# Kernel optimization log

Measured on AMD Instinct MI355X. Metric: run time of the kernel, lower is better.

Reference implementation:

```python
import jax, jax.numpy as jnp
import numpy as np
import math

N_EMBD = 1024
DIM_ATT = 1024
N_LAYER = 24
LAYER_ID = 12
B, T = 4, 4096


def _init_params():
    r01 = LAYER_ID / (N_LAYER - 1)
    r1a0 = 1.0 - LAYER_ID / N_LAYER
    ddd = np.arange(N_EMBD, dtype=np.float32) / N_EMBD
    h = np.arange(DIM_ATT, dtype=np.float32)
    decay_speed = -5.0 + 8.0 * (h / (DIM_ATT - 1)) ** (0.7 + 1.3 * r01)
    zigzag = (((np.arange(DIM_ATT) + 1) % 3) - 1).astype(np.float32) * 0.5
    time_first = np.float32(math.log(0.3)) + zigzag
    return {
        'time_decay': jnp.asarray(decay_speed, jnp.float32),
        'time_first': jnp.asarray(time_first, jnp.float32),
        'time_mix_k': jnp.asarray(ddd ** r1a0, jnp.float32),
        'time_mix_v': jnp.asarray(ddd ** r1a0 + 0.3 * r01, jnp.float32),
        'time_mix_r': jnp.asarray(ddd ** (0.5 * r1a0), jnp.float32),
    }


def setup_inputs() -> dict:
    key = jax.random.key(0)
    ks = jax.random.split(key, 5)
    inp = {'x': jax.random.normal(ks[0], (B, T, N_EMBD), jnp.float32)}
    inp.update(_init_params())
    s = 1.0 / math.sqrt(N_EMBD)
    inp['Wk'] = jax.random.normal(ks[1], (DIM_ATT, N_EMBD), jnp.float32) * s
    inp['Wv'] = jax.random.normal(ks[2], (DIM_ATT, N_EMBD), jnp.float32) * s
    inp['Wr'] = jax.random.normal(ks[3], (DIM_ATT, N_EMBD), jnp.float32) * s
    inp['Wo'] = jax.random.normal(ks[4], (N_EMBD, DIM_ATT), jnp.float32) * (1.0 / math.sqrt(DIM_ATT))
    return inp


def _wkv(w, u, k, v):
    # Numerically stable RWKV-4 WKV recurrence. w = -exp(time_decay) <= 0.
    # k, v: [B, T, C]; w, u: [C]. Scan over T with [B, C] state.
    def step(carry, kv):
        aa, bb, pp = carry
        kt, vt = kv
        ww = u + kt
        p = jnp.maximum(pp, ww)
        e1 = jnp.exp(pp - p)
        e2 = jnp.exp(ww - p)
        y = (e1 * aa + e2 * vt) / (e1 * bb + e2)
        ww2 = pp + w
        p2 = jnp.maximum(ww2, kt)
        e1b = jnp.exp(ww2 - p2)
        e2b = jnp.exp(kt - p2)
        return (e1b * aa + e2b * vt, e1b * bb + e2b, p2), y

    Bb, Tt, C = k.shape
    init = (jnp.zeros((Bb, C), k.dtype), jnp.zeros((Bb, C), k.dtype),
            jnp.full((Bb, C), -1e38, k.dtype))
    _, ys = jax.lax.scan(step, init, (jnp.swapaxes(k, 0, 1), jnp.swapaxes(v, 0, 1)))
    return jnp.swapaxes(ys, 0, 1)


def reference(x, time_decay, time_first, time_mix_k, time_mix_v, time_mix_r, Wk, Wv, Wr, Wo):
    # time_shift: ZeroPad2d((0,0,1,-1)) -> shift right by 1 along T with zero fill
    xx = jnp.pad(x, ((0, 0), (1, 0), (0, 0)))[:, :-1]
    xk = x * time_mix_k + xx * (1.0 - time_mix_k)
    xv = x * time_mix_v + xx * (1.0 - time_mix_v)
    xr = x * time_mix_r + xx * (1.0 - time_mix_r)
    k = jnp.einsum('btc,dc->btd', xk, Wk)
    v = jnp.einsum('btc,dc->btd', xv, Wv)
    sr = jax.nn.sigmoid(jnp.einsum('btc,dc->btd', xr, Wr))
    w = -jnp.exp(time_decay)  # as in the WKV CUDA kernel
    rwkv = sr * _wkv(w, time_first, k, v)
    return jnp.einsum('btd,cd->btc', rwkv, Wo)
```

## Files before the change

kernel.cpp:

```cpp
#include <hip/hip_runtime.h>
#include <hip/hip_bf16.h>
#include <stdint.h>

#define B_ 4
#define T_ 4096
#define C_ 1024
#define D_ 1024
#define NC_ 64
#define LC_ 64

typedef __bf16 bf16x8 __attribute__((ext_vector_type(8)));
typedef float  f32x4  __attribute__((ext_vector_type(4)));

__device__ __forceinline__ unsigned short f2bf(float f) {
    union { float f; unsigned u; } c; c.f = f;
    return (unsigned short)((c.u + 0x7fffu + ((c.u >> 16) & 1u)) >> 16);
}

__device__ __forceinline__ void gload_lds16(const unsigned short* g, unsigned short* l) {
    __builtin_amdgcn_global_load_lds(
        (const __attribute__((address_space(1))) void*)g,
        (__attribute__((address_space(3))) void*)l,
        16, 0, 0);
}

__global__ void cast_bf16_kernel(const float* __restrict__ s, unsigned short* __restrict__ d) {
    int i = blockIdx.x * blockDim.x + threadIdx.x;
    float4 v = *reinterpret_cast<const float4*>(s + ((size_t)i << 2));
    ushort4 o;
    o.x = f2bf(v.x); o.y = f2bf(v.y); o.z = f2bf(v.z); o.w = f2bf(v.w);
    *reinterpret_cast<ushort4*>(d + ((size_t)i << 2)) = o;
}

__global__ void mix_cast_kernel(const float* __restrict__ x,
                                const float* __restrict__ mk,
                                const float* __restrict__ mv,
                                const float* __restrict__ mr,
                                unsigned short* __restrict__ xk,
                                unsigned short* __restrict__ xv,
                                unsigned short* __restrict__ xr) {
    int i = blockIdx.x * blockDim.x + threadIdx.x;
    int base = i << 2;
    int c = base & (C_ - 1);
    int m = base >> 10;
    int t = m & (T_ - 1);
    float4 xc = *reinterpret_cast<const float4*>(x + base);
    float4 xp = make_float4(0.f, 0.f, 0.f, 0.f);
    if (t != 0) xp = *reinterpret_cast<const float4*>(x + base - C_);
    float4 k4 = *reinterpret_cast<const float4*>(mk + c);
    float4 v4 = *reinterpret_cast<const float4*>(mv + c);
    float4 r4 = *reinterpret_cast<const float4*>(mr + c);
    ushort4 ok, ov, orr;
    ok.x  = f2bf(xp.x + k4.x * (xc.x - xp.x));
    ok.y  = f2bf(xp.y + k4.y * (xc.y - xp.y));
    ok.z  = f2bf(xp.z + k4.z * (xc.z - xp.z));
    ok.w  = f2bf(xp.w + k4.w * (xc.w - xp.w));
    ov.x  = f2bf(xp.x + v4.x * (xc.x - xp.x));
    ov.y  = f2bf(xp.y + v4.y * (xc.y - xp.y));
    ov.z  = f2bf(xp.z + v4.z * (xc.z - xp.z));
    ov.w  = f2bf(xp.w + v4.w * (xc.w - xp.w));
    orr.x = f2bf(xp.x + r4.x * (xc.x - xp.x));
    orr.y = f2bf(xp.y + r4.y * (xc.y - xp.y));
    orr.z = f2bf(xp.z + r4.z * (xc.z - xp.z));
    orr.w = f2bf(xp.w + r4.w * (xc.w - xp.w));
    *reinterpret_cast<ushort4*>(xk + base) = ok;
    *reinterpret_cast<ushort4*>(xv + base) = ov;
    *reinterpret_cast<ushort4*>(xr + base) = orr;
}

template<bool SIG>
__global__ __launch_bounds__(256) void gemm_bt(const unsigned short* __restrict__ A,
                                               const unsigned short* __restrict__ Bw,
                                               float* __restrict__ Cm) {
    __shared__ __align__(16) unsigned short As[128 * 32];
    __shared__ __align__(16) unsigned short Bs[128 * 32];
    const int tid  = threadIdx.x;
    const int lane = tid & 63;
    const int wid  = tid >> 6;
    const int xcd   = blockIdx.x & 7;
    const int local = blockIdx.x >> 3;
    const int bm = (((xcd << 4) + (local >> 3))) << 7;
    const int bn = (local & 7) << 7;
    const int wr = (wid >> 1) * 64;
    const int wc = (wid & 1) * 64;

    f32x4 acc[4][4] = {};

    const int r0 = tid >> 2;
    const int ck = (tid & 3) * 8;
    const unsigned short* ga0 = A  + (size_t)(bm + r0) * 1024 + ck;
    const unsigned short* gb0 = Bw + (size_t)(bn + r0) * 1024 + ck;
    const unsigned short* ga1 = ga0 + (size_t)64 * 1024;
    const unsigned short* gb1 = gb0 + (size_t)64 * 1024;
    unsigned short* lA0 = As + wid * 512;
    unsigned short* lA1 = As + 2048 + wid * 512;
    unsigned short* lB0 = Bs + wid * 512;
    unsigned short* lB1 = Bs + 2048 + wid * 512;

    const int arow = wr + (lane & 15);
    const int brow = wc + (lane & 15);
    const int ko   = (lane >> 4) * 8;

    for (int ks = 0; ks < 32; ++ks) {
        __syncthreads();
        gload_lds16(ga0, lA0);
        gload_lds16(ga1, lA1);
        gload_lds16(gb0, lB0);
        gload_lds16(gb1, lB1);
        ga0 += 32; ga1 += 32; gb0 += 32; gb1 += 32;
        asm volatile("s_waitcnt vmcnt(0)" ::: "memory");
        __syncthreads();

        bf16x8 af[4], bfr[4];
        #pragma unroll
        for (int i = 0; i < 4; ++i) {
            af[i]  = *reinterpret_cast<const bf16x8*>(&As[(arow + i * 16) * 32 + ko]);
            bfr[i] = *reinterpret_cast<const bf16x8*>(&Bs[(brow + i * 16) * 32 + ko]);
        }
        #pragma unroll
        for (int i = 0; i < 4; ++i)
            #pragma unroll
            for (int j = 0; j < 4; ++j)
                acc[i][j] = __builtin_amdgcn_mfma_f32_16x16x32_bf16(af[i], bfr[j], acc[i][j], 0, 0, 0);
    }

    const int row0 = bm + wr + (lane >> 4) * 4;
    const int col0 = bn + wc + (lane & 15);
    #pragma unroll
    for (int i = 0; i < 4; ++i)
        #pragma unroll
        for (int j = 0; j < 4; ++j)
            #pragma unroll
            for (int r = 0; r < 4; ++r) {
                float vv = acc[i][j][r];
                if (SIG) vv = 1.0f / (1.0f + __expf(-vv));
                Cm[(size_t)(row0 + i * 16 + r) * 1024 + col0 + j * 16] = vv;
            }
}

__global__ void wkv_chunk(const float* __restrict__ k, const float* __restrict__ v,
                          const float* __restrict__ td,
                          float* __restrict__ ca, float* __restrict__ cb, float* __restrict__ cp,
                          int NB) {
    int gid = blockIdx.x * 256 + threadIdx.x;
    int d   = gid & (D_ - 1);
    int rem = gid >> 10;
    int j   = rem & (NC_ - 1);
    int b   = rem >> 6;
    float w = -__expf(td[d]);
    size_t base = ((size_t)(b * T_ + j * LC_)) * D_ + d;
    float aa = 0.f, bb = 0.f, pp = -1e38f;
    for (int t = 0; t < LC_; ++t) {
        float kt = k[base + (size_t)t * D_];
        float vt = v[base + (size_t)t * D_];
        float ww = pp + w;
        float p  = fmaxf(ww, kt);
        float e1 = __expf(ww - p);
        float e2 = __expf(kt - p);
        aa = e1 * aa + e2 * vt;
        bb = e1 * bb + e2;
        pp = p;
    }
    int ch  = (b << 10) + d;
    int idx = j * (NB << 10) + ch;
    ca[idx] = aa;
    cb[idx] = bb;
    cp[idx] = pp;
}

__global__ void wkv_scan(const float* __restrict__ ca, const float* __restrict__ cb,
                         const float* __restrict__ cp, const float* __restrict__ td,
                         float* __restrict__ sa, float* __restrict__ sb, float* __restrict__ sp,
                         int NB) {
    int ch = blockIdx.x * 256 + threadIdx.x;
    int d  = ch & (D_ - 1);
    float w  = -__expf(td[d]);
    float wL = w * (float)LC_;
    float A = 0.f, Bv = 0.f, P = -1e38f;
    int stride = NB << 10;
    for (int j = 0; j < NC_; ++j) {
        int idx = j * stride + ch;
        sa[idx] = A; sb[idx] = Bv; sp[idx] = P;
        float a2 = ca[idx], b2 = cb[idx], p2 = cp[idx];
        float Pd = P + wL;
        float pm = fmaxf(Pd, p2);
        float e1 = __expf(Pd - pm);
        float e2 = __expf(p2 - pm);
        A  = e1 * A  + e2 * a2;
        Bv = e1 * Bv + e2 * b2;
        P  = pm;
    }
}

__global__ void wkv_emit(const float* __restrict__ k, const float* __restrict__ v,
                         const float* __restrict__ sr, const float* __restrict__ td,
                         const float* __restrict__ tf,
                         const float* __restrict__ sa, const float* __restrict__ sb,
                         const float* __restrict__ sp,
                         unsigned short* __restrict__ ybf, int NB) {
    int gid = blockIdx.x * 256 + threadIdx.x;
    int d   = gid & (D_ - 1);
    int rem = gid >> 10;
    int j   = rem & (NC_ - 1);
    int b   = rem >> 6;
    int ch  = (b << 10) + d;
    float w = -__expf(td[d]);
    float u = tf[d];
    int idx = j * (NB << 10) + ch;
    float aa = sa[idx], bb = sb[idx], pp = sp[idx];
    size_t base = ((size_t)(b * T_ + j * LC_)) * D_ + d;
    for (int t = 0; t < LC_; ++t) {
        size_t o = base + (size_t)t * D_;
        float kt = k[o];
        float vt = v[o];
        float ww = u + kt;
        float p  = fmaxf(pp, ww);
        float e1 = __expf(pp - p);
        float e2 = __expf(ww - p);
        float y  = (e1 * aa + e2 * vt) / (e1 * bb + e2);
        ybf[o] = f2bf(sr[o] * y);
        float ww2 = pp + w;
        float p2  = fmaxf(ww2, kt);
        float e1b = __expf(ww2 - p2);
        float e2b = __expf(kt - p2);
        aa = e1b * aa + e2b * vt;
        bb = e1b * bb + e2b;
        pp = p2;
    }
}

extern "C" void kernel_launch(void* const* d_in, const int* in_sizes, int n_in,
                              void* d_out, int out_size, void* d_ws, size_t ws_size,
                              hipStream_t stream) {
    const float* x  = (const float*)d_in[0];
    const float* td = (const float*)d_in[1];
    const float* tf = (const float*)d_in[2];
    const float* mk = (const float*)d_in[3];
    const float* mv = (const float*)d_in[4];
    const float* mr = (const float*)d_in[5];
    const float* Wk = (const float*)d_in[6];
    const float* Wv = (const float*)d_in[7];
    const float* Wr = (const float*)d_in[8];
    const float* Wo = (const float*)d_in[9];
    float* out = (float*)d_out;

    char* ws = (char*)d_ws;
    unsigned short* wkbf = (unsigned short*)(ws + ((size_t)0 << 20));
    unsigned short* wvbf = (unsigned short*)(ws + ((size_t)2 << 20));
    unsigned short* wrbf = (unsigned short*)(ws + ((size_t)4 << 20));
    unsigned short* wobf = (unsigned short*)(ws + ((size_t)6 << 20));

    cast_bf16_kernel<<<1024, 256, 0, stream>>>(Wk, wkbf);
    cast_bf16_kernel<<<1024, 256, 0, stream>>>(Wv, wvbf);
    cast_bf16_kernel<<<1024, 256, 0, stream>>>(Wr, wrbf);
    cast_bf16_kernel<<<1024, 256, 0, stream>>>(Wo, wobf);

    if (ws_size >= ((size_t)240 << 20)) {
        unsigned short* xk = (unsigned short*)(ws + ((size_t)8  << 20));
        unsigned short* xv = (unsigned short*)(ws + ((size_t)40 << 20));
        unsigned short* xr = (unsigned short*)(ws + ((size_t)72 << 20));
        float* kb  = (float*)(ws + ((size_t)104 << 20));
        float* vb  = (float*)(ws + ((size_t)168 << 20));
        float* srb = (float*)(ws + ((size_t)8   << 20));
        unsigned short* ybf = xr;
        float* ca = (float*)(ws + ((size_t)232 << 20));
        float* cb = ca + (1u << 18);
        float* cp = cb + (1u << 18);
        float* sa = cp + (1u << 18);
        float* sb = sa + (1u << 18);
        float* sp = sb + (1u << 18);

        mix_cast_kernel<<<16384, 256, 0, stream>>>(x, mk, mv, mr, xk, xv, xr);
        gemm_bt<false><<<1024, 256, 0, stream>>>(xk, wkbf, kb);
        gemm_bt<false><<<1024, 256, 0, stream>>>(xv, wvbf, vb);
        gemm_bt<true ><<<1024, 256, 0, stream>>>(xr, wrbf, srb);
        wkv_chunk<<<1024, 256, 0, stream>>>(kb, vb, td, ca, cb, cp, 4);
        wkv_scan<<<16, 256, 0, stream>>>(ca, cb, cp, td, sa, sb, sp, 4);
        wkv_emit<<<1024, 256, 0, stream>>>(kb, vb, srb, td, tf, sa, sb, sp, ybf, 4);
        gemm_bt<false><<<1024, 256, 0, stream>>>(ybf, wobf, out);
    } else {
        unsigned short* xk = (unsigned short*)(ws + ((size_t)8  << 20));
        unsigned short* xv = (unsigned short*)(ws + ((size_t)16 << 20));
        unsigned short* xr = (unsigned short*)(ws + ((size_t)24 << 20));
        float* kb  = (float*)(ws + ((size_t)32 << 20));
        float* vb  = (float*)(ws + ((size_t)48 << 20));
        float* srb = (float*)(ws + ((size_t)64 << 20));
        float* ca  = (float*)(ws + ((size_t)80 << 20));
        float* cb  = ca + (1u << 16);
        float* cp  = cb + (1u << 16);
        float* sa  = cp + (1u << 16);
        float* sb  = sa + (1u << 16);
        float* sp  = sb + (1u << 16);
        unsigned short* ybf = xk;

        for (int b = 0; b < B_; ++b) {
            const float* xb = x + (size_t)b * T_ * C_;
            float* outb = out + (size_t)b * T_ * C_;
            mix_cast_kernel<<<4096, 256, 0, stream>>>(xb, mk, mv, mr, xk, xv, xr);
            gemm_bt<false><<<256, 256, 0, stream>>>(xk, wkbf, kb);
            gemm_bt<false><<<256, 256, 0, stream>>>(xv, wvbf, vb);
            gemm_bt<true ><<<256, 256, 0, stream>>>(xr, wrbf, srb);
            wkv_chunk<<<256, 256, 0, stream>>>(kb, vb, td, ca, cb, cp, 1);
            wkv_scan<<<4, 256, 0, stream>>>(ca, cb, cp, td, sa, sb, sp, 1);
            wkv_emit<<<256, 256, 0, stream>>>(kb, vb, srb, td, tf, sa, sb, sp, ybf, 1);
            gemm_bt<false><<<256, 256, 0, stream>>>(ybf, wobf, outb);
        }
    }
}
```

Before: 472.5 us.

## Double-buffer GEMM LDS tiles and XOR-swizzle K chunks to cut bank conflicts

```diff
diff --git a/kernel.cpp b/kernel.cpp
--- a/kernel.cpp
+++ b/kernel.cpp
@@ -72,14 +72,14 @@
 __global__ __launch_bounds__(256) void gemm_bt(const unsigned short* __restrict__ A,
                                                const unsigned short* __restrict__ Bw,
                                                float* __restrict__ Cm) {
-    __shared__ __align__(16) unsigned short As[128 * 32];
-    __shared__ __align__(16) unsigned short Bs[128 * 32];
+    __shared__ __align__(16) unsigned short As[2][4096];
+    __shared__ __align__(16) unsigned short Bs[2][4096];
     const int tid  = threadIdx.x;
     const int lane = tid & 63;
     const int wid  = tid >> 6;
     const int xcd   = blockIdx.x & 7;
     const int local = blockIdx.x >> 3;
-    const int bm = (((xcd << 4) + (local >> 3))) << 7;
+    const int bm = ((xcd << 4) + (local >> 3)) << 7;
     const int bn = (local & 7) << 7;
     const int wr = (wid >> 1) * 64;
     const int wc = (wid & 1) * 64;
@@ -87,41 +87,50 @@
     f32x4 acc[4][4] = {};
 
     const int r0 = tid >> 2;
-    const int ck = (tid & 3) * 8;
+    const int sw = (r0 & 3) ^ ((r0 >> 2) & 3);
+    const int ck = (((tid & 3) ^ sw) * 8);
     const unsigned short* ga0 = A  + (size_t)(bm + r0) * 1024 + ck;
     const unsigned short* gb0 = Bw + (size_t)(bn + r0) * 1024 + ck;
     const unsigned short* ga1 = ga0 + (size_t)64 * 1024;
     const unsigned short* gb1 = gb0 + (size_t)64 * 1024;
-    unsigned short* lA0 = As + wid * 512;
-    unsigned short* lA1 = As + 2048 + wid * 512;
-    unsigned short* lB0 = Bs + wid * 512;
-    unsigned short* lB1 = Bs + 2048 + wid * 512;
+    const int wofs = wid * 512;
 
     const int arow = wr + (lane & 15);
     const int brow = wc + (lane & 15);
-    const int ko   = (lane >> 4) * 8;
-
+    const int sr   = (lane & 3) ^ ((lane >> 2) & 3);
+    const int ko   = (((lane >> 4) ^ sr) * 8);
+
+    gload_lds16(ga0, &As[0][wofs]);
+    gload_lds16(ga1, &As[0][2048 + wofs]);
+    gload_lds16(gb0, &Bs[0][wofs]);
+    gload_lds16(gb1, &Bs[0][2048 + wofs]);
+    ga0 += 32; ga1 += 32; gb0 += 32; gb1 += 32;
+    asm volatile("s_waitcnt vmcnt(0)" ::: "memory");
+    __builtin_amdgcn_s_barrier();
+
+    int cur = 0;
     for (int ks = 0; ks < 32; ++ks) {
-        __syncthreads();
-        gload_lds16(ga0, lA0);
-        gload_lds16(ga1, lA1);
-        gload_lds16(gb0, lB0);
-        gload_lds16(gb1, lB1);
-        ga0 += 32; ga1 += 32; gb0 += 32; gb1 += 32;
-        asm volatile("s_waitcnt vmcnt(0)" ::: "memory");
-        __syncthreads();
-
+        if (ks < 31) {
+            gload_lds16(ga0, &As[cur ^ 1][wofs]);
+            gload_lds16(ga1, &As[cur ^ 1][2048 + wofs]);
+            gload_lds16(gb0, &Bs[cur ^ 1][wofs]);
+            gload_lds16(gb1, &Bs[cur ^ 1][2048 + wofs]);
+            ga0 += 32; ga1 += 32; gb0 += 32; gb1 += 32;
+        }
         bf16x8 af[4], bfr[4];
         #pragma unroll
         for (int i = 0; i < 4; ++i) {
-            af[i]  = *reinterpret_cast<const bf16x8*>(&As[(arow + i * 16) * 32 + ko]);
-            bfr[i] = *reinterpret_cast<const bf16x8*>(&Bs[(brow + i * 16) * 32 + ko]);
+            af[i]  = *reinterpret_cast<const bf16x8*>(&As[cur][(arow + i * 16) * 32 + ko]);
+            bfr[i] = *reinterpret_cast<const bf16x8*>(&Bs[cur][(brow + i * 16) * 32 + ko]);
         }
         #pragma unroll
         for (int i = 0; i < 4; ++i)
             #pragma unroll
             for (int j = 0; j < 4; ++j)
                 acc[i][j] = __builtin_amdgcn_mfma_f32_16x16x32_bf16(af[i], bfr[j], acc[i][j], 0, 0, 0);
+        asm volatile("s_waitcnt vmcnt(0)" ::: "memory");
+        __builtin_amdgcn_s_barrier();
+        cur ^= 1;
     }
 
     const int row0 = bm + wr + (lane >> 4) * 4;
```

Result: faster. 459.1 us (-2.8%).
